# Performance work log

Measured on AMD Instinct MI355X. Metric: run time of the kernel, lower is better.

## Reference

```python
import jax, jax.numpy as jnp
import numpy as np

T_SCALES = [0.0, 0.25, 0.5, 0.75, 1.0]  # ODEblock time_scales; Euler step per consecutive pair
NUM_ZEROS = 10
BETA = 0.6  # defined in ODEFunc but unused in its forward


def _odefunc(x, x0, adj, alpha, w, d, w2, d2):
    # x: [B, N, T, Fa]; adj: [N, N]; alpha: [N]; w: [Fa, Fa]; d: [Fa]; w2: [T, T]; d2: [T]
    a = jax.nn.sigmoid(alpha)[None, :, None, None]              # [1, N, 1, 1]
    xa = jnp.einsum('ij,kjln->kiln', adj, x)                    # adjacency propagation over nodes
    dc = jnp.clip(d, 0.0, 1.0)
    W = (w * dc) @ w.T                                          # [Fa, Fa]
    # NOTE: faithful to torch source: 'ijkl,mn->ijkm' has NO shared contraction
    # index => xw = (sum_l x) outer (sum_n W) — reproduced exactly.
    xw = jnp.einsum('ijkl,mn->ijkm', x, W)
    d2c = jnp.clip(d2, 0.0, 1.0)
    W2 = (w2 * d2c) @ w2.T                                      # [T, T]
    xw2 = jnp.einsum('ijkl,kn->ijnl', x, W2)                    # temporal mixing
    # f = alpha/2*xa - x + xw - x + xw2 - x + x0
    return a * 0.5 * xa - 3.0 * x + xw + xw2 + x0


def setup_inputs() -> dict:
    key = jax.random.key(0)
    k1, k2 = jax.random.split(key)
    B, N, T, F = 32, 512, 24, 64
    Fa = F + NUM_ZEROS
    x = jax.random.normal(k1, (B, N, T, F), dtype=jnp.float32)
    adj = jax.random.uniform(k2, (N, N), dtype=jnp.float32) / N  # normalized dense adjacency
    alpha = 0.8 * jnp.ones((N,), jnp.float32)                    # nn.Parameter init 0.8*ones
    w = jnp.eye(Fa, dtype=jnp.float32)                           # nn.Parameter init eye
    d = jnp.ones((Fa,), jnp.float32)                             # nn.Parameter init ones
    w2 = jnp.eye(T, dtype=jnp.float32)
    d2 = jnp.ones((T,), jnp.float32)
    return {"x": x, "adj": adj, "alpha": alpha, "w": w, "d": d, "w2": w2, "d2": d2}


def reference(x, adj, alpha, w, d, w2, d2):
    B, N, T, F = x.shape
    if F == 64:
        x_aug = jnp.concatenate(
            [x, jnp.zeros((B, N, T, NUM_ZEROS), dtype=x.dtype)], axis=3)
    else:
        x_aug = x
    x0 = jax.lax.stop_gradient(x_aug)  # set_x0 uses clone().detach()
    # Euler odeint with two time points does one step: z = x + dt * f(x).
    # Original loop restarts from x_aug each iteration, so f is constant.
    f = _odefunc(x_aug, x0, adj, alpha, w, d, w2, d2)
    z = x_aug
    for i in range(len(T_SCALES) - 1):
        dt = T_SCALES[i + 1] - T_SCALES[i]
        z = x_aug + dt * f  # overwrites z each iteration, as in the torch code
    return jax.nn.relu(z)
```

## Files before the change

kernel.cpp:

```cpp
#include <hip/hip_runtime.h>
#include <hip/hip_bf16.h>
#include <cstdint>
#include <cstddef>

#define B_  32
#define N_  512
#define T_  24
#define F_  64
#define FA_ 74
#define NC  1536
#define NCF 1776

typedef __attribute__((ext_vector_type(8))) short short8;
typedef __attribute__((ext_vector_type(4))) float floatx4;

#define WS_ADJ  1536
#define WS_XT   132608
#define WS_E    12715520
#define WS_BYTES_NEEDED (27264512ULL * 4ULL)

#define AS1(p) ((const __attribute__((address_space(1))) void*)(p))
#define AS3(p) ((__attribute__((address_space(3))) void*)(p))

__device__ __forceinline__ unsigned short f2b(float v) {
  __hip_bfloat16 h = __float2bfloat16(v);
  return *(unsigned short*)&h;
}
__device__ __forceinline__ float b2f(unsigned short u) {
  return __uint_as_float(((unsigned)u) << 16);
}

__global__ __launch_bounds__(256) void params_kernel(
    const float* __restrict__ alpha, const float* __restrict__ w,
    const float* __restrict__ d, const float* __restrict__ w2,
    const float* __restrict__ d2, float* __restrict__ ws) {
  __shared__ float cs[FA_];
  int tid = threadIdx.x;
  if (tid < FA_) {
    float s = 0.f;
    for (int n = 0; n < FA_; ++n) s += w[n * FA_ + tid];
    cs[tid] = s;
  }
  __syncthreads();
  if (tid < FA_) {
    float s = 0.f;
    for (int p = 0; p < FA_; ++p) {
      float dc = fminf(fmaxf(d[p], 0.f), 1.f);
      s += w[tid * FA_ + p] * dc * cs[p];
    }
    ws[tid] = s;
  }
  for (int e = tid; e < T_ * T_; e += 256) {
    int a = e / T_, b = e % T_;
    float s = 0.f;
    for (int p = 0; p < T_; ++p) {
      float dc = fminf(fmaxf(d2[p], 0.f), 1.f);
      s += w2[a * T_ + p] * dc * w2[b * T_ + p];
    }
    ws[128 + e] = s;
  }
  for (int i = tid; i < N_; i += 256) ws[768 + i] = 1.f / (1.f + __expf(-alpha[i]));
}

__global__ __launch_bounds__(256) void convert_adj_kernel(
    const float* __restrict__ adj, float* __restrict__ ws) {
  unsigned short* adjM = (unsigned short*)(ws + WS_ADJ);
  int g = (blockIdx.x * 256 + threadIdx.x) * 4;
  int i = g >> 9;
  float s = 0.125f * ws[768 + i];
  float4 v = *(const float4*)&adj[g];
  ushort4 u;
  u.x = f2b(s * v.x); u.y = f2b(s * v.y); u.z = f2b(s * v.z); u.w = f2b(s * v.w);
  *(ushort4*)&adjM[g] = u;
}

template <bool EPATH>
__global__ __launch_bounds__(256) void prep_kernel(
    const float* __restrict__ x, float* __restrict__ ws, float* __restrict__ out) {
  __shared__ __align__(16) unsigned short xsh[16 * NC];
  __shared__ __align__(16) float ebuf[4 * NCF];
  unsigned short* eh = (unsigned short*)ebuf;

  int tid = threadIdx.x;
  int b = blockIdx.y;
  int i0 = blockIdx.x * 16;
  const float* xb = x + ((size_t)(b * N_ + i0)) * NC;

#pragma unroll
  for (int it = 0; it < 24; ++it) {
    int g = it * 256 + tid;
    float4 v = *(const float4*)&xb[g * 4];
    ushort4 u;
    u.x = f2b(v.x); u.y = f2b(v.y); u.z = f2b(v.z); u.w = f2b(v.w);
    *(ushort4*)&xsh[g * 4] = u;
  }
  __syncthreads();

  unsigned short* xT = (unsigned short*)(ws + WS_XT) + (size_t)b * NC * 512;
#pragma unroll
  for (int j = 0; j < 6; ++j) {
    int c = j * 256 + tid;
    unsigned vv[8];
#pragma unroll
    for (int k2 = 0; k2 < 8; ++k2) {
      unsigned lo = xsh[(2 * k2) * NC + c];
      unsigned hi = xsh[(2 * k2 + 1) * NC + c];
      vv[k2] = lo | (hi << 16);
    }
    uint4 w0; w0.x = vv[0]; w0.y = vv[1]; w0.z = vv[2]; w0.w = vv[3];
    uint4 w1; w1.x = vv[4]; w1.y = vv[5]; w1.z = vv[6]; w1.w = vv[7];
    *(uint4*)&xT[(size_t)c * 512 + i0] = w0;
    *(uint4*)&xT[(size_t)c * 512 + i0 + 8] = w1;
  }

  int wave = tid >> 6, lane = tid & 63;
  const float* __restrict__ W2p = ws + 128;
  float rsw4 = 0.25f * ws[lane];
  float rswA = (lane < 10) ? 0.25f * ws[64 + lane] : 0.f;

  for (int p = 0; p < 4; ++p) {
    int node = p * 4 + wave;
    float xcol[24];
#pragma unroll
    for (int t = 0; t < 24; ++t) xcol[t] = b2f(xsh[node * NC + t * 64 + lane]);
    float S[24];
#pragma unroll
    for (int t = 0; t < 24; ++t) S[t] = xcol[t];
#pragma unroll
    for (int off = 32; off >= 1; off >>= 1) {
#pragma unroll
      for (int t = 0; t < 24; ++t) S[t] += __shfl_xor(S[t], off, 64);
    }
    float accv[24];
#pragma unroll
    for (int to = 0; to < 24; ++to) {
      float a = 0.f;
#pragma unroll
      for (int tp = 0; tp < 24; ++tp) a += xcol[tp] * W2p[to * 24 + tp];
      accv[to] = a;
    }
#pragma unroll
    for (int t = 0; t < 24; ++t) {
      float ev = 0.5f * xcol[t] + 0.25f * accv[t] + S[t] * rsw4;
      if (EPATH) eh[wave * NCF + t * 74 + lane] = f2b(ev);
      else       ebuf[wave * NCF + t * 74 + lane] = ev;
    }
#pragma unroll
    for (int t = 0; t < 24; ++t) {
      if (lane < 10) {
        float av = fmaxf(S[t] * rswA, 0.f);
        if (EPATH) eh[wave * NCF + t * 74 + 64 + lane] = f2b(av);
        else       ebuf[wave * NCF + t * 74 + 64 + lane] = av;
      }
    }
    __syncthreads();
    if (EPATH) {
      unsigned short* Eg = (unsigned short*)(ws + WS_E) +
                           ((size_t)(b * N_ + i0 + p * 4)) * NCF;
      const uint4* src = (const uint4*)eh;
      uint4* dst = (uint4*)Eg;
#pragma unroll
      for (int j = 0; j < 4; ++j) {
        int idx = j * 256 + tid;
        if (idx < 888) dst[idx] = src[idx];
      }
      float* ob = out + ((size_t)(b * N_ + i0 + p * 4)) * NCF;
#pragma unroll
      for (int j = 0; j < 4; ++j) {
        int e = j * 256 + tid;
        if (e < 960) {
          int nd = e / 240, rem = e - nd * 240;
          int t = rem / 10, m = rem - t * 10;
          ob[(size_t)nd * NCF + t * 74 + 64 + m] = b2f(eh[nd * NCF + t * 74 + 64 + m]);
        }
      }
    } else {
      float* og = out + ((size_t)(b * N_ + i0 + p * 4)) * NCF;
#pragma unroll
      for (int j = 0; j < 7; ++j) {
        int idx = j * 256 + tid;
        if (idx < 1776) ((float4*)og)[idx] = ((const float4*)ebuf)[idx];
      }
    }
    __syncthreads();
  }
}

template <bool EPATH>
__global__ __launch_bounds__(256) void gemm_kernel(
    const float* __restrict__ ws, float* __restrict__ out) {
  const unsigned short* adjM = (const unsigned short*)(ws + WS_ADJ);
  const unsigned short* xT   = (const unsigned short*)(ws + WS_XT);
  __shared__ short As[128 * 32];
  __shared__ short Bs[128 * 32];

  int tid = threadIdx.x;
  int b  = blockIdx.z;
  int i0 = blockIdx.y * 128;
  int c0 = blockIdx.x * 128;
  int wave = tid >> 6, lane = tid & 63;
  int mw = (wave & 1) * 64, nw = (wave >> 1) * 64;
  int l15 = lane & 15, l4 = lane >> 4;

  floatx4 acc[4][4];
#pragma unroll
  for (int mt = 0; mt < 4; ++mt)
#pragma unroll
    for (int nt = 0; nt < 4; ++nt) acc[mt][nt] = (floatx4){0.f, 0.f, 0.f, 0.f};

  const size_t bRow = (size_t)b * NC;
  for (int k0 = 0; k0 < 512; k0 += 32) {
#pragma unroll
    for (int rep = 0; rep < 2; ++rep) {
      int chunk = rep * 256 + tid;
      int r = chunk >> 2;
      int k8 = (chunk & 3) * 8;
      __builtin_amdgcn_global_load_lds(AS1(adjM + (size_t)(i0 + r) * 512 + k0 + k8),
                                       AS3(&As[chunk * 8]), 16, 0, 0);
      __builtin_amdgcn_global_load_lds(AS1(xT + (bRow + c0 + r) * 512 + k0 + k8),
                                       AS3(&Bs[chunk * 8]), 16, 0, 0);
    }
    __syncthreads();

    short8 af[4], bf[4];
#pragma unroll
    for (int mt = 0; mt < 4; ++mt)
      af[mt] = *(const short8*)&As[(mw + mt * 16 + l15) * 32 + l4 * 8];
#pragma unroll
    for (int nt = 0; nt < 4; ++nt)
      bf[nt] = *(const short8*)&Bs[(nw + nt * 16 + l15) * 32 + l4 * 8];
#pragma unroll
    for (int mt = 0; mt < 4; ++mt)
#pragma unroll
      for (int nt = 0; nt < 4; ++nt)
        acc[mt][nt] = __builtin_amdgcn_mfma_f32_16x16x32_bf16(af[mt], bf[nt], acc[mt][nt], 0, 0, 0);
    __syncthreads();
  }

  const unsigned short* Eb = (const unsigned short*)(ws + WS_E) + (size_t)b * N_ * NCF;
#pragma unroll
  for (int mt = 0; mt < 4; ++mt) {
#pragma unroll
    for (int nt = 0; nt < 4; ++nt) {
      int col = c0 + nw + nt * 16 + l15;
      int t = col >> 6, f = col & 63;
      int cofs = t * 74 + f;
#pragma unroll
      for (int r = 0; r < 4; ++r) {
        int row = i0 + mw + mt * 16 + l4 * 4 + r;
        size_t o = (size_t)(b * N_ + row) * NCF + cofs;
        float val;
        if (EPATH) val = acc[mt][nt][r] + b2f(Eb[(size_t)row * NCF + cofs]);
        else       val = out[o] + acc[mt][nt][r];
        out[o] = fmaxf(val, 0.f);
      }
    }
  }
}

extern "C" void kernel_launch(void* const* d_in, const int* in_sizes, int n_in,
                              void* d_out, int out_size, void* d_ws, size_t ws_size,
                              hipStream_t stream) {
  const float* x     = (const float*)d_in[0];
  const float* adj   = (const float*)d_in[1];
  const float* alpha = (const float*)d_in[2];
  const float* w     = (const float*)d_in[3];
  const float* d     = (const float*)d_in[4];
  const float* w2    = (const float*)d_in[5];
  const float* d2    = (const float*)d_in[6];
  float* out = (float*)d_out;
  float* ws  = (float*)d_ws;

  hipLaunchKernelGGL(params_kernel, dim3(1), dim3(256), 0, stream,
                     alpha, w, d, w2, d2, ws);
  hipLaunchKernelGGL(convert_adj_kernel, dim3(256), dim3(256), 0, stream, adj, ws);

  if (ws_size >= WS_BYTES_NEEDED) {
    hipLaunchKernelGGL((prep_kernel<true>), dim3(32, 32), dim3(256), 0, stream, x, ws, out);
    hipLaunchKernelGGL((gemm_kernel<true>), dim3(12, 4, B_), dim3(256), 0, stream, ws, out);
  } else {
    hipLaunchKernelGGL((prep_kernel<false>), dim3(32, 32), dim3(256), 0, stream, x, ws, out);
    hipLaunchKernelGGL((gemm_kernel<false>), dim3(12, 4, B_), dim3(256), 0, stream, ws, out);
  }
}
```

Baseline: 391.8 us.

## Use k-slab layout for transposed x and halve prep tile size

The transposed bf16 copy of x now lives in k-major slabs of 8 nodes, so each prep block writes whole contiguous 16-byte runs instead of scattered strided stores. The GEMM B-tile loads and LDS fragment addressing are changed to read this slab layout. Prep blocks now cover 8 nodes instead of 16, which cuts shared memory per block, doubles the grid and adds an occupancy hint. The risk is that GEMM global loads become less contiguous per row, and the ebuf size and p-loop changes have to stay consistent with the hidden epilogue code.

```diff
diff --git a/kernel.cpp b/kernel.cpp
--- a/kernel.cpp
+++ b/kernel.cpp
@@ -75,19 +75,20 @@
 }
 
 template <bool EPATH>
-__global__ __launch_bounds__(256) void prep_kernel(
+__global__ __launch_bounds__(256, 4) void prep_kernel(
     const float* __restrict__ x, float* __restrict__ ws, float* __restrict__ out) {
-  __shared__ __align__(16) unsigned short xsh[16 * NC];
-  __shared__ __align__(16) float ebuf[4 * NCF];
+  __shared__ __align__(16) unsigned short xsh[8 * NC];
+  __shared__ __align__(16) float ebuf[EPATH ? 2 * NCF : 4 * NCF];
   unsigned short* eh = (unsigned short*)ebuf;
 
   int tid = threadIdx.x;
   int b = blockIdx.y;
-  int i0 = blockIdx.x * 16;
+  int kb = blockIdx.x;
+  int i0 = kb * 8;
   const float* xb = x + ((size_t)(b * N_ + i0)) * NC;
 
 #pragma unroll
-  for (int it = 0; it < 24; ++it) {
+  for (int it = 0; it < 12; ++it) {
     int g = it * 256 + tid;
     float4 v = *(const float4*)&xb[g * 4];
     ushort4 u;
@@ -96,21 +97,26 @@
   }
   __syncthreads();
 
-  unsigned short* xT = (unsigned short*)(ws + WS_XT) + (size_t)b * NC * 512;
-#pragma unroll
-  for (int j = 0; j < 6; ++j) {
-    int c = j * 256 + tid;
-    unsigned vv[8];
-#pragma unroll
-    for (int k2 = 0; k2 < 8; ++k2) {
-      unsigned lo = xsh[(2 * k2) * NC + c];
-      unsigned hi = xsh[(2 * k2 + 1) * NC + c];
-      vv[k2] = lo | (hi << 16);
-    }
-    uint4 w0; w0.x = vv[0]; w0.y = vv[1]; w0.z = vv[2]; w0.w = vv[3];
-    uint4 w1; w1.x = vv[4]; w1.y = vv[5]; w1.z = vv[6]; w1.w = vv[7];
-    *(uint4*)&xT[(size_t)c * 512 + i0] = w0;
-    *(uint4*)&xT[(size_t)c * 512 + i0 + 8] = w1;
+  {
+    unsigned short* xTs = (unsigned short*)(ws + WS_XT) + ((size_t)(b * 64 + kb)) * (NC * 8);
+#pragma unroll
+    for (int j = 0; j < 3; ++j) {
+      int cp = j * 256 + tid;
+      unsigned u[8];
+#pragma unroll
+      for (int k = 0; k < 8; ++k) u[k] = *(const unsigned*)&xsh[k * NC + cp * 2];
+      uint4 w0, w1;
+      w0.x = (u[0] & 0xffffu) | (u[1] << 16);
+      w0.y = (u[2] & 0xffffu) | (u[3] << 16);
+      w0.z = (u[4] & 0xffffu) | (u[5] << 16);
+      w0.w = (u[6] & 0xffffu) | (u[7] << 16);
+      w1.x = (u[0] >> 16) | (u[1] & 0xffff0000u);
+      w1.y = (u[2] >> 16) | (u[3] & 0xffff0000u);
+      w1.z = (u[4] >> 16) | (u[5] & 0xffff0000u);
+      w1.w = (u[6] >> 16) | (u[7] & 0xffff0000u);
+      *(uint4*)&xTs[(size_t)cp * 16] = w0;
+      *(uint4*)&xTs[(size_t)cp * 16 + 8] = w1;
+    }
   }
 
   int wave = tid >> 6, lane = tid & 63;
@@ -118,7 +124,7 @@
   float rsw4 = 0.25f * ws[lane];
   float rswA = (lane < 10) ? 0.25f * ws[64 + lane] : 0.f;
 
-  for (int p = 0; p < 4; ++p) {
+  for (int p = 0; p < 2; ++p) {
     int node = p * 4 + wave;
     float xcol[24];
 #pragma unroll
@@ -192,7 +198,7 @@
   const unsigned short* adjM = (const unsigned short*)(ws + WS_ADJ);
   const unsigned short* xT   = (const unsigned short*)(ws + WS_XT);
   __shared__ short As[128 * 32];
-  __shared__ short Bs[128 * 32];
+  __shared__ short Bs[4 * 128 * 8];
 
   int tid = threadIdx.x;
   int b  = blockIdx.z;
@@ -208,17 +214,19 @@
 #pragma unroll
     for (int nt = 0; nt < 4; ++nt) acc[mt][nt] = (floatx4){0.f, 0.f, 0.f, 0.f};
 
-  const size_t bRow = (size_t)b * NC;
+  const size_t slabBase = (size_t)b * 64;
   for (int k0 = 0; k0 < 512; k0 += 32) {
+    int kb0 = k0 >> 3;
 #pragma unroll
     for (int rep = 0; rep < 2; ++rep) {
       int chunk = rep * 256 + tid;
-      int r = chunk >> 2;
-      int k8 = (chunk & 3) * 8;
+      int r = chunk >> 2, k8 = (chunk & 3) * 8;
       __builtin_amdgcn_global_load_lds(AS1(adjM + (size_t)(i0 + r) * 512 + k0 + k8),
                                        AS3(&As[chunk * 8]), 16, 0, 0);
-      __builtin_amdgcn_global_load_lds(AS1(xT + (bRow + c0 + r) * 512 + k0 + k8),
-                                       AS3(&Bs[chunk * 8]), 16, 0, 0);
+      int rr = chunk >> 7, c = chunk & 127;
+      __builtin_amdgcn_global_load_lds(
+          AS1(xT + ((slabBase + kb0 + rr) * NC + c0 + c) * 8),
+          AS3(&Bs[rr * 1024 + c * 8]), 16, 0, 0);
     }
     __syncthreads();
 
@@ -228,7 +236,7 @@
       af[mt] = *(const short8*)&As[(mw + mt * 16 + l15) * 32 + l4 * 8];
 #pragma unroll
     for (int nt = 0; nt < 4; ++nt)
-      bf[nt] = *(const short8*)&Bs[(nw + nt * 16 + l15) * 32 + l4 * 8];
+      bf[nt] = *(const short8*)&Bs[l4 * 1024 + (nw + nt * 16 + l15) * 8];
 #pragma unroll
     for (int mt = 0; mt < 4; ++mt)
 #pragma unroll
@@ -276,10 +284,10 @@
   hipLaunchKernelGGL(convert_adj_kernel, dim3(256), dim3(256), 0, stream, adj, ws);
 
   if (ws_size >= WS_BYTES_NEEDED) {
-    hipLaunchKernelGGL((prep_kernel<true>), dim3(32, 32), dim3(256), 0, stream, x, ws, out);
+    hipLaunchKernelGGL((prep_kernel<true>), dim3(64, 32), dim3(256), 0, stream, x, ws, out);
     hipLaunchKernelGGL((gemm_kernel<true>), dim3(12, 4, B_), dim3(256), 0, stream, ws, out);
   } else {
-    hipLaunchKernelGGL((prep_kernel<false>), dim3(32, 32), dim3(256), 0, stream, x, ws, out);
+    hipLaunchKernelGGL((prep_kernel<false>), dim3(64, 32), dim3(256), 0, stream, x, ws, out);
     hipLaunchKernelGGL((gemm_kernel<false>), dim3(12, 4, B_), dim3(256), 0, stream, ws, out);
   }
 }
```

Result: faster. 377.1 us (-3.7%).
